# Kernel tuning notes

Measured on AMD Instinct MI355X. Metric: run time of the kernel, lower is better.

The kernel has to match this reference:

```python
import jax, jax.numpy as jnp
import numpy as np

C = 512
GROUPS = 8
EPS = 1e-5


def setup_inputs() -> dict:
    key = jax.random.key(0)
    ks = jax.random.split(key, 7)
    B, H, W = 16, 32, 32
    x = jax.random.normal(ks[0], (B, C, H, W), dtype=jnp.float32)
    # GroupNorm affine params
    gn_scale = jnp.ones((C,), jnp.float32)
    gn_bias = jnp.zeros((C,), jnp.float32)
    # 1x1 convs == channel matmuls
    s_qkv = 1.0 / np.sqrt(C)
    qkv_w = jax.random.uniform(ks[1], (3 * C, C), jnp.float32, -s_qkv, s_qkv)
    qkv_b = jax.random.uniform(ks[2], (3 * C,), jnp.float32, -s_qkv, s_qkv)
    proj_w = jax.random.uniform(ks[3], (C, C), jnp.float32, -s_qkv, s_qkv)
    proj_b = jax.random.uniform(ks[4], (C,), jnp.float32, -s_qkv, s_qkv)
    return {"x": x, "gn_scale": gn_scale, "gn_bias": gn_bias,
            "qkv_w": qkv_w, "qkv_b": qkv_b, "proj_w": proj_w, "proj_b": proj_b}


def _group_norm(x, scale, bias):
    B, c, H, W = x.shape
    xg = x.reshape(B, GROUPS, c // GROUPS, H, W)
    mean = xg.mean(axis=(2, 3, 4), keepdims=True)
    var = xg.var(axis=(2, 3, 4), keepdims=True)
    xn = ((xg - mean) * jax.lax.rsqrt(var + EPS)).reshape(B, c, H, W)
    return xn * scale[None, :, None, None] + bias[None, :, None, None]


def reference(x, gn_scale, gn_bias, qkv_w, qkv_b, proj_w, proj_b):
    B, c, H, W = x.shape
    N = H * W
    h = _group_norm(x, gn_scale, gn_bias)            # [B,C,H,W]
    hf = h.reshape(B, c, N)                          # flatten spatial
    qkv = jnp.einsum('oc,bcn->bon', qkv_w, hf) + qkv_b[None, :, None]  # [B,3C,N]
    q, k, v = jnp.split(qkv, 3, axis=1)              # each [B,C,N]
    attn = jnp.einsum('bci,bcj->bij', q, k) * (c ** -0.5)  # [B,N,N]
    attn = jax.nn.softmax(attn, axis=2)
    out = jnp.einsum('bij,bcj->bci', attn, v)        # [B,C,N]
    out = jnp.einsum('oc,bcn->bon', proj_w, out) + proj_b[None, :, None]
    return out.reshape(B, c, H, W) + x
```

## Files before the change

kernel.cpp:

```cpp
#include <hip/hip_runtime.h>

typedef __bf16 bf16x8 __attribute__((ext_vector_type(8)));
typedef float f32x4 __attribute__((ext_vector_type(4)));
typedef unsigned short u16;

__device__ __forceinline__ u16 f2bf(float f) {
  unsigned u = __float_as_uint(f);
  u += 0x7fffu + ((u >> 16) & 1u);
  return (u16)(u >> 16);
}
__device__ __forceinline__ float bf2f(u16 h) {
  return __uint_as_float(((unsigned)h) << 16);
}

#define GLOAD_LDS(g, l)                                              \
  __builtin_amdgcn_global_load_lds(                                  \
      (const __attribute__((address_space(1))) void*)(g),            \
      (__attribute__((address_space(3))) void*)(l), 16, 0, 0)

template <int K>
__device__ __forceinline__ void gemm_core_s(const u16* __restrict__ Ab,
                                            const u16* __restrict__ Bb,
                                            f32x4 acc[4][4]) {
  __shared__ __align__(16) u16 As[2][8192], Bs[2][8192];
  const int tid = threadIdx.x;
  const int wave = tid >> 6, lane = tid & 63;
  const int sr = tid >> 3;
  const int sc = ((tid ^ sr) & 7) << 3;
  const u16* ag = Ab + (size_t)sr * K + sc;
  const u16* bg = Bb + (size_t)sr * K + sc;
  const int ldst = tid * 8;
  const int wr = (wave >> 1) << 6, wc = (wave & 1) << 6;
  const int lrow = lane & 15, klane = lane >> 4;
  const int rx = lrow & 7;
  const int ao = (wr + lrow) * 64 + ((klane ^ rx) << 3);
  const int bo = (wc + lrow) * 64 + ((klane ^ rx) << 3);

  const u16 *a_cur = As[0] + ldst, *a_nxt = As[1] + ldst;
  const u16 *b_cur = Bs[0] + ldst, *b_nxt = Bs[1] + ldst;
  const u16 *ar = As[0], *br = Bs[0];
  const u16 *an = As[1], *bn = Bs[1];

#pragma unroll
  for (int r = 0; r < 4; r++) GLOAD_LDS(ag + (size_t)(r * 32) * K, a_cur + r * 2048);
#pragma unroll
  for (int r = 0; r < 4; r++) GLOAD_LDS(bg + (size_t)(r * 32) * K, b_cur + r * 2048);
  __syncthreads();

  for (int k = 64; k < K; k += 64) {
#pragma unroll
    for (int r = 0; r < 4; r++) GLOAD_LDS(ag + (size_t)(r * 32) * K + k, a_nxt + r * 2048);
#pragma unroll
    for (int r = 0; r < 4; r++) GLOAD_LDS(bg + (size_t)(r * 32) * K + k, b_nxt + r * 2048);
#pragma unroll
    for (int half = 0; half < 2; half++) {
      const int xo = half << 5;
      bf16x8 a[4], b[4];
#pragma unroll
      for (int i = 0; i < 4; i++) a[i] = *(const bf16x8*)(ar + ((ao ^ xo) + (i << 10)));
#pragma unroll
      for (int i = 0; i < 4; i++) b[i] = *(const bf16x8*)(br + ((bo ^ xo) + (i << 10)));
#pragma unroll
      for (int mi = 0; mi < 4; mi++)
#pragma unroll
        for (int ni = 0; ni < 4; ni++)
          acc[mi][ni] = __builtin_amdgcn_mfma_f32_16x16x32_bf16(a[mi], b[ni], acc[mi][ni], 0, 0, 0);
    }
    __syncthreads();
    const u16* t;
    t = a_cur; a_cur = a_nxt; a_nxt = t;
    t = b_cur; b_cur = b_nxt; b_nxt = t;
    t = ar; ar = an; an = t;
    t = br; br = bn; bn = t;
  }
#pragma unroll
  for (int half = 0; half < 2; half++) {
    const int xo = half << 5;
    bf16x8 a[4], b[4];
#pragma unroll
    for (int i = 0; i < 4; i++) a[i] = *(const bf16x8*)(ar + ((ao ^ xo) + (i << 10)));
#pragma unroll
    for (int i = 0; i < 4; i++) b[i] = *(const bf16x8*)(br + ((bo ^ xo) + (i << 10)));
#pragma unroll
    for (int mi = 0; mi < 4; mi++)
#pragma unroll
      for (int ni = 0; ni < 4; ni++)
        acc[mi][ni] = __builtin_amdgcn_mfma_f32_16x16x32_bf16(a[mi], b[ni], acc[mi][ni], 0, 0, 0);
  }
}

#define ACC_INIT                                     \
  f32x4 acc[4][4];                                   \
  {                                                  \
    const f32x4 _z = {0.f, 0.f, 0.f, 0.f};           \
    _Pragma("unroll")                                \
    for (int _i = 0; _i < 4; _i++)                   \
      _Pragma("unroll")                              \
      for (int _j = 0; _j < 4; _j++) acc[_i][_j] = _z; \
  }

#define EPI_SETUP                                                            \
  const int tid = threadIdx.x;                                               \
  const int wave = tid >> 6;                                                 \
  const int lane = tid & 63;                                                 \
  const int mb = (blockIdx.y << 7) + ((wave >> 1) << 6) + (((lane >> 4) & 3) << 2); \
  const int nb = (blockIdx.x << 7) + ((wave & 1) << 6) + (lane & 15);

__global__ void __launch_bounds__(256) k_convw(const float* __restrict__ qw,
                                               const float* __restrict__ pw,
                                               u16* __restrict__ wq, u16* __restrict__ wp) {
  const int t = blockIdx.x * 256 + threadIdx.x;
  for (int i = t; i < 786432; i += 262144) wq[i] = f2bf(qw[i]);
  wp[t] = f2bf(pw[t]);
}

__global__ void __launch_bounds__(256) k_gn(const float* __restrict__ x,
                                            const float* __restrict__ gsc,
                                            const float* __restrict__ gbi,
                                            u16* __restrict__ h) {
  const int b = blockIdx.x >> 3, g = blockIdx.x & 7;
  const size_t xoff = ((size_t)b * 512 + g * 64) * 1024;
  const float* xb = x + xoff;
  const int tid = threadIdx.x;
  const int wave = tid >> 6, lane = tid & 63;

  float s1 = 0.f, s2 = 0.f;
  const float4* xb4 = (const float4*)xb;
  for (int i = tid; i < 16384; i += 256) {
    float4 v = xb4[i];
    s1 += v.x + v.y + v.z + v.w;
    s2 += v.x * v.x + v.y * v.y + v.z * v.z + v.w * v.w;
  }
#pragma unroll
  for (int off = 32; off; off >>= 1) { s1 += __shfl_xor(s1, off); s2 += __shfl_xor(s2, off); }
  __shared__ float red[8];
  if (lane == 0) { red[wave] = s1; red[4 + wave] = s2; }
  __syncthreads();
  const float t1 = red[0] + red[1] + red[2] + red[3];
  const float t2 = red[4] + red[5] + red[6] + red[7];
  const float mean = t1 * (1.f / 65536.f);
  const float rstd = rsqrtf(t2 * (1.f / 65536.f) - mean * mean + 1e-5f);

  __shared__ u16 tile[64][66];
  for (int chunk = 0; chunk < 16; chunk++) {
    const int n0 = chunk << 6;
    __syncthreads();
#pragma unroll
    for (int r = 0; r < 16; r++) {
      const int cl = (r << 2) + wave;
      const int ch = (g << 6) + cl;
      float v = xb[(size_t)cl * 1024 + n0 + lane];
      float o = (v - mean) * rstd * gsc[ch] + gbi[ch];
      tile[lane][cl] = f2bf(o);
    }
    __syncthreads();
#pragma unroll
    for (int r = 0; r < 16; r++) {
      const int nl = (r << 2) + wave;
      h[((size_t)b * 1024 + n0 + nl) * 512 + (g << 6) + lane] = tile[nl][lane];
    }
  }
}

__global__ void __launch_bounds__(256) k_qkv(const u16* __restrict__ W,
                                             const u16* __restrict__ h,
                                             const float* __restrict__ bias,
                                             u16* __restrict__ qt, u16* __restrict__ kt,
                                             u16* __restrict__ vv) {
  const int b = blockIdx.z;
  ACC_INIT
  gemm_core_s<512>(W + ((size_t)blockIdx.y << 7) * 512,
                   h + ((size_t)b << 19) + (((size_t)blockIdx.x << 7) * 512), acc);
  EPI_SETUP
  const int sel = blockIdx.y >> 2;
  const float scale = 0.044194173824159216f;
  if (sel < 2) {
    u16* dst = sel ? kt : qt;
    const float sc = sel ? 1.f : scale;
    const int obase = mb - sel * 512;
#pragma unroll
    for (int mi = 0; mi < 4; mi++) {
      const int o = mb + mi * 16;
#pragma unroll
      for (int ni = 0; ni < 4; ni++) {
        const int n = nb + ni * 16;
        ushort4 pk;
        pk.x = f2bf((acc[mi][ni][0] + bias[o + 0]) * sc);
        pk.y = f2bf((acc[mi][ni][1] + bias[o + 1]) * sc);
        pk.z = f2bf((acc[mi][ni][2] + bias[o + 2]) * sc);
        pk.w = f2bf((acc[mi][ni][3] + bias[o + 3]) * sc);
        *(ushort4*)(dst + ((size_t)b * 1024 + n) * 512 + (obase + mi * 16)) = pk;
      }
    }
  } else {
#pragma unroll
    for (int mi = 0; mi < 4; mi++) {
      const int o = mb + mi * 16;
#pragma unroll
      for (int ni = 0; ni < 4; ni++) {
        const int n = nb + ni * 16;
#pragma unroll
        for (int r = 0; r < 4; r++) {
          float val = acc[mi][ni][r] + bias[o + r];
          vv[((size_t)b * 512 + (o - 1024 + r)) * 1024 + n] = f2bf(val);
        }
      }
    }
  }
}

__global__ void __launch_bounds__(256) k_sgemm(const u16* __restrict__ qt,
                                               const u16* __restrict__ kt,
                                               u16* __restrict__ S) {
  const int b = blockIdx.z;
  ACC_INIT
  gemm_core_s<512>(qt + ((size_t)b << 19) + ((size_t)blockIdx.y << 7) * 512,
                   kt + ((size_t)b << 19) + ((size_t)blockIdx.x << 7) * 512, acc);
  EPI_SETUP
  const size_t base = (size_t)b << 20;
#pragma unroll
  for (int mi = 0; mi < 4; mi++)
#pragma unroll
    for (int ni = 0; ni < 4; ni++) {
      const int j = nb + ni * 16;
#pragma unroll
      for (int r = 0; r < 4; r++)
        S[base + (size_t)(mb + mi * 16 + r) * 1024 + j] = f2bf(acc[mi][ni][r]);
    }
}

__global__ void __launch_bounds__(256) k_softmax(u16* __restrict__ S) {
  const size_t base = (((size_t)blockIdx.y << 10) + blockIdx.x) << 10;
  const int tid = threadIdx.x;
  const int wave = tid >> 6, lane = tid & 63;
  ushort4 raw = *(const ushort4*)(S + base + tid * 4);
  float v0 = bf2f(raw.x), v1 = bf2f(raw.y), v2 = bf2f(raw.z), v3 = bf2f(raw.w);
  float m = fmaxf(fmaxf(v0, v1), fmaxf(v2, v3));
#pragma unroll
  for (int off = 32; off; off >>= 1) m = fmaxf(m, __shfl_xor(m, off));
  __shared__ float s1[4], s2[4];
  if (lane == 0) s1[wave] = m;
  __syncthreads();
  m = fmaxf(fmaxf(s1[0], s1[1]), fmaxf(s1[2], s1[3]));
  v0 = __expf(v0 - m); v1 = __expf(v1 - m); v2 = __expf(v2 - m); v3 = __expf(v3 - m);
  float s = v0 + v1 + v2 + v3;
#pragma unroll
  for (int off = 32; off; off >>= 1) s += __shfl_xor(s, off);
  if (lane == 0) s2[wave] = s;
  __syncthreads();
  s = s2[0] + s2[1] + s2[2] + s2[3];
  const float inv = 1.0f / s;
  raw.x = f2bf(v0 * inv); raw.y = f2bf(v1 * inv);
  raw.z = f2bf(v2 * inv); raw.w = f2bf(v3 * inv);
  *(ushort4*)(S + base + tid * 4) = raw;
}

__global__ void __launch_bounds__(256) k_ogemm(const u16* __restrict__ vv,
                                               const u16* __restrict__ P,
                                               u16* __restrict__ ot) {
  const int b = blockIdx.z;
  ACC_INIT
  gemm_core_s<1024>(vv + ((size_t)b << 19) + ((size_t)blockIdx.y << 7) * 1024,
                    P + ((size_t)b << 20) + ((size_t)blockIdx.x << 7) * 1024, acc);
  EPI_SETUP
#pragma unroll
  for (int mi = 0; mi < 4; mi++) {
    const int c = mb + mi * 16;
#pragma unroll
    for (int ni = 0; ni < 4; ni++) {
      const int i = nb + ni * 16;
      ushort4 pk;
      pk.x = f2bf(acc[mi][ni][0]);
      pk.y = f2bf(acc[mi][ni][1]);
      pk.z = f2bf(acc[mi][ni][2]);
      pk.w = f2bf(acc[mi][ni][3]);
      *(ushort4*)(ot + ((size_t)b << 19) + (size_t)i * 512 + c) = pk;
    }
  }
}

__global__ void __launch_bounds__(256) k_proj(const u16* __restrict__ W,
                                              const u16* __restrict__ ot,
                                              const float* __restrict__ pb,
                                              const float* __restrict__ x,
                                              float* __restrict__ out) {
  const int b = blockIdx.z;
  ACC_INIT
  gemm_core_s<512>(W + ((size_t)blockIdx.y << 7) * 512,
                   ot + ((size_t)b << 19) + ((size_t)blockIdx.x << 7) * 512, acc);
  EPI_SETUP
#pragma unroll
  for (int mi = 0; mi < 4; mi++) {
    const int o = mb + mi * 16;
#pragma unroll
    for (int ni = 0; ni < 4; ni++) {
      const int n = nb + ni * 16;
      const size_t base = ((size_t)b * 512 + o) * 1024 + n;
#pragma unroll
      for (int r = 0; r < 4; r++)
        out[base + (size_t)r * 1024] = acc[mi][ni][r] + pb[o + r] + x[base + (size_t)r * 1024];
    }
  }
}

extern "C" void kernel_launch(void* const* d_in, const int* in_sizes, int n_in,
                              void* d_out, int out_size, void* d_ws, size_t ws_size,
                              hipStream_t stream) {
  const float* x     = (const float*)d_in[0];
  const float* gsc   = (const float*)d_in[1];
  const float* gbi   = (const float*)d_in[2];
  const float* qkvw  = (const float*)d_in[3];
  const float* qkvb  = (const float*)d_in[4];
  const float* projw = (const float*)d_in[5];
  const float* projb = (const float*)d_in[6];
  float* out = (float*)d_out;

  char* ws = (char*)d_ws;
  u16* wq = (u16*)(ws);
  u16* wp = (u16*)(ws + 1572864);
  u16* h  = (u16*)(ws + 2097152);
  u16* qt = (u16*)(ws + 18874368);
  u16* kt = (u16*)(ws + 35651584);
  u16* vv = (u16*)(ws + 52428864);
  u16* S  = (u16*)(ws + 69206080);
  u16* ot = h;

  k_convw<<<1024, 256, 0, stream>>>(qkvw, projw, wq, wp);
  k_gn<<<128, 256, 0, stream>>>(x, gsc, gbi, h);
  k_qkv<<<dim3(8, 12, 16), 256, 0, stream>>>(wq, h, qkvb, qt, kt, vv);
  k_sgemm<<<dim3(8, 8, 16), 256, 0, stream>>>(qt, kt, S);
  k_softmax<<<dim3(1024, 16), 256, 0, stream>>>(S);
  k_ogemm<<<dim3(8, 4, 16), 256, 0, stream>>>(vv, S, ot);
  k_proj<<<dim3(8, 4, 16), 256, 0, stream>>>(wp, ot, projb, x, out);
}
```

Measured before the change: 268.5 us.

## Split GroupNorm into partial-stats, finalize, and normalize kernels for more parallelism

Replaces the single 128-block GroupNorm kernel with three kernels: 512 blocks compute partial sums over quarter-groups, a tiny kernel finalizes mean and rstd per group, and 1024 blocks apply normalization and transpose to bf16. This spreads the reduction and normalize/transpose over many more blocks to fill the GPU's compute units. In exchange it adds two extra kernel launches and reads x twice from memory (already done before). The stats scratch reuses the S workspace region before S is written.

```diff
diff --git a/kernel.cpp b/kernel.cpp
--- a/kernel.cpp
+++ b/kernel.cpp
@@ -114,44 +114,60 @@
   wp[t] = f2bf(pw[t]);
 }
 
-__global__ void __launch_bounds__(256) k_gn(const float* __restrict__ x,
-                                            const float* __restrict__ gsc,
-                                            const float* __restrict__ gbi,
-                                            u16* __restrict__ h) {
-  const int b = blockIdx.x >> 3, g = blockIdx.x & 7;
-  const size_t xoff = ((size_t)b * 512 + g * 64) * 1024;
-  const float* xb = x + xoff;
-  const int tid = threadIdx.x;
-  const int wave = tid >> 6, lane = tid & 63;
-
+__global__ void __launch_bounds__(256) k_gn1(const float* __restrict__ x,
+                                             float* __restrict__ part) {
+  const int blk = blockIdx.x;
+  const float4* src = (const float4*)(x + ((size_t)(blk >> 2) * 64 + (blk & 3) * 16) * 1024);
   float s1 = 0.f, s2 = 0.f;
-  const float4* xb4 = (const float4*)xb;
-  for (int i = tid; i < 16384; i += 256) {
-    float4 v = xb4[i];
+  for (int i = threadIdx.x; i < 4096; i += 256) {
+    float4 v = src[i];
     s1 += v.x + v.y + v.z + v.w;
     s2 += v.x * v.x + v.y * v.y + v.z * v.z + v.w * v.w;
   }
 #pragma unroll
   for (int off = 32; off; off >>= 1) { s1 += __shfl_xor(s1, off); s2 += __shfl_xor(s2, off); }
   __shared__ float red[8];
+  const int wave = threadIdx.x >> 6, lane = threadIdx.x & 63;
   if (lane == 0) { red[wave] = s1; red[4 + wave] = s2; }
   __syncthreads();
-  const float t1 = red[0] + red[1] + red[2] + red[3];
-  const float t2 = red[4] + red[5] + red[6] + red[7];
-  const float mean = t1 * (1.f / 65536.f);
-  const float rstd = rsqrtf(t2 * (1.f / 65536.f) - mean * mean + 1e-5f);
-
+  if (threadIdx.x == 0) {
+    part[blk * 2]     = red[0] + red[1] + red[2] + red[3];
+    part[blk * 2 + 1] = red[4] + red[5] + red[6] + red[7];
+  }
+}
+
+__global__ void __launch_bounds__(128) k_gn1b(const float* __restrict__ part,
+                                              float* __restrict__ stats) {
+  const int g = threadIdx.x;
+  const float s1 = part[g * 8 + 0] + part[g * 8 + 2] + part[g * 8 + 4] + part[g * 8 + 6];
+  const float s2 = part[g * 8 + 1] + part[g * 8 + 3] + part[g * 8 + 5] + part[g * 8 + 7];
+  const float mean = s1 * (1.f / 65536.f);
+  const float var = s2 * (1.f / 65536.f) - mean * mean;
+  stats[g * 2]     = mean;
+  stats[g * 2 + 1] = rsqrtf(var + 1e-5f);
+}
+
+__global__ void __launch_bounds__(256) k_gn2(const float* __restrict__ x,
+                                             const float* __restrict__ gsc,
+                                             const float* __restrict__ gbi,
+                                             const float* __restrict__ stats,
+                                             u16* __restrict__ h) {
+  const int chunk = blockIdx.x & 7, g = (blockIdx.x >> 3) & 7, b = blockIdx.x >> 6;
+  const int bg = b * 8 + g;
+  const float mean = stats[bg * 2], rstd = stats[bg * 2 + 1];
+  const float* xb = x + ((size_t)b * 512 + g * 64) * 1024;
+  const int tid = threadIdx.x, wave = tid >> 6, lane = tid & 63;
   __shared__ u16 tile[64][66];
-  for (int chunk = 0; chunk < 16; chunk++) {
-    const int n0 = chunk << 6;
-    __syncthreads();
+#pragma unroll
+  for (int half = 0; half < 2; half++) {
+    const int n0 = chunk * 128 + half * 64;
+    if (half) __syncthreads();
 #pragma unroll
     for (int r = 0; r < 16; r++) {
       const int cl = (r << 2) + wave;
       const int ch = (g << 6) + cl;
       float v = xb[(size_t)cl * 1024 + n0 + lane];
-      float o = (v - mean) * rstd * gsc[ch] + gbi[ch];
-      tile[lane][cl] = f2bf(o);
+      tile[lane][cl] = f2bf((v - mean) * rstd * gsc[ch] + gbi[ch]);
     }
     __syncthreads();
 #pragma unroll
@@ -324,9 +340,13 @@
   u16* vv = (u16*)(ws + 52428864);
   u16* S  = (u16*)(ws + 69206080);
   u16* ot = h;
+  float* part  = (float*)(ws + 69206080);
+  float* stats = (float*)(ws + 69206080 + 8192);
 
   k_convw<<<1024, 256, 0, stream>>>(qkvw, projw, wq, wp);
-  k_gn<<<128, 256, 0, stream>>>(x, gsc, gbi, h);
+  k_gn1<<<512, 256, 0, stream>>>(x, part);
+  k_gn1b<<<1, 128, 0, stream>>>(part, stats);
+  k_gn2<<<1024, 256, 0, stream>>>(x, gsc, gbi, stats, h);
   k_qkv<<<dim3(8, 12, 16), 256, 0, stream>>>(wq, h, qkvb, qt, kt, vv);
   k_sgemm<<<dim3(8, 8, 16), 256, 0, stream>>>(qt, kt, S);
   k_softmax<<<dim3(1024, 16), 256, 0, stream>>>(S);
```

New measurement: 250.6 us. -6.6%, faster.
